# Optimization experiments

Hardware: AMD Instinct MI355X
Metric: run time of the kernel (lower is better)

The kernel has to match this reference:

```python
import jax, jax.numpy as jnp
import numpy as np

NUM_BITS = 8
MAX_INT = 2 ** (NUM_BITS - 1) - 1   # 127
MIN_INT = -2 ** (NUM_BITS - 1) - 1  # -129 (faithful to source)


def setup_inputs() -> dict:
    key = jax.random.key(0)
    k1, k2 = jax.random.split(key)
    B, H, S, D = 2, 16, 2048, 128
    score = jax.random.normal(k1, (B, H, S, S), dtype=jnp.float32)
    value = jax.random.normal(k2, (B, H, S, D), dtype=jnp.float32)
    query_scale = jnp.array([0.05], dtype=jnp.float32)
    key_scale = jnp.array([0.02], dtype=jnp.float32)
    return {"score": score, "value": value,
            "query_scale": query_scale, "key_scale": key_scale}


def _fake_quant(x, scale):
    # round(x/scale) then clamp to [MIN_INT, MAX_INT]
    return jnp.clip(jnp.round(x / scale), MIN_INT, MAX_INT)


def reference(score, value, query_scale, key_scale):
    # score: [B,H,S,S], value: [B,H,S,D]
    score_int = _fake_quant(score, query_scale)
    value_int = _fake_quant(value, key_scale)
    # integer-valued matmul (done in float here, as in the torch source)
    output_int = jnp.einsum('bhsk,bhkd->bhsd', score_int, value_int)
    final_scale = query_scale * key_scale
    return output_int * final_scale
```

## Files before the change

### kernel.cpp

```cpp
#include <hip/hip_runtime.h>
#include <hip/hip_bf16.h>
#include <stdint.h>

#define S_DIM 2048
#define D_DIM 128
#define BH_N  32
#define BM    64
#define BK    64
#define ASTR  72

typedef float  f32x4  __attribute__((ext_vector_type(4)));
typedef unsigned int u32x2 __attribute__((ext_vector_type(2)));
typedef unsigned int u32x4 __attribute__((ext_vector_type(4)));
typedef short  bf16x8 __attribute__((ext_vector_type(8)));

__device__ __forceinline__ unsigned short quant1(float v, float inv) {
    float q = rintf(v * inv);
    q = fminf(fmaxf(q, -129.0f), 127.0f);
    return (unsigned short)(__float_as_uint(q) >> 16);
}

__global__ __launch_bounds__(256) void vt_quant_kernel(
        const float* __restrict__ value,
        const float* __restrict__ ks_p,
        unsigned short* __restrict__ vt) {
    __shared__ unsigned short T[D_DIM * ASTR];

    const int bid = blockIdx.x;
    const int bh  = bid >> 5;
    const int k0  = (bid & 31) * BK;
    const float inv = 1.0f / ks_p[0];
    const int tid = threadIdx.x;

    const float* src = value + ((size_t)bh * S_DIM + k0) * D_DIM;

#pragma unroll
    for (int i = 0; i < 8; ++i) {
        int f  = tid + 256 * i;
        int k  = f >> 5;
        int c4 = (f & 31) * 4;
        f32x4 v = *(const f32x4*)(src + (size_t)k * D_DIM + c4);
        T[(c4 + 0) * ASTR + k] = quant1(v.x, inv);
        T[(c4 + 1) * ASTR + k] = quant1(v.y, inv);
        T[(c4 + 2) * ASTR + k] = quant1(v.z, inv);
        T[(c4 + 3) * ASTR + k] = quant1(v.w, inv);
    }
    __syncthreads();

    unsigned short* dst = vt + (size_t)bh * D_DIM * S_DIM + k0;
#pragma unroll
    for (int i = 0; i < 4; ++i) {
        int c = tid + 256 * i;
        int n = c >> 3;
        int q = (c & 7) * 8;
        u32x4 x = *(const u32x4*)(&T[n * ASTR + q]);
        *(u32x4*)(dst + (size_t)n * S_DIM + q) = x;
    }
}

__global__ __launch_bounds__(256, 4) void bmm_kernel(
        const float* __restrict__ score,
        const unsigned short* __restrict__ vt,
        const float* __restrict__ qs_p,
        const float* __restrict__ ks_p,
        float* __restrict__ out) {
    __shared__ unsigned short As[BM * ASTR];
    __shared__ unsigned short Bs[D_DIM * BK];

    const int bid = blockIdx.x;
    const int bh  = bid >> 5;
    const int m0  = (bid & 31) * BM;

    const float qs  = qs_p[0];
    const float inv_qs = 1.0f / qs;
    const float fin = qs * ks_p[0];

    const int tid  = threadIdx.x;
    const int lane = tid & 63;
    const int wave = tid >> 6;
    const int wm   = (wave >> 1) * 32;
    const int wn   = (wave & 1) * 64;
    const int m16  = lane & 15;
    const int quad = lane >> 4;

    const float* A = score + (size_t)bh * S_DIM * S_DIM + (size_t)m0 * S_DIM;
    const unsigned short* Bt = vt + (size_t)bh * D_DIM * S_DIM;

    f32x4 acc[2][4] = {};

    for (int kb = 0; kb < S_DIM; kb += BK) {
#pragma unroll
        for (int i = 0; i < 4; ++i) {
            int p  = i * 256 + tid;
            int n  = p >> 3;
            int ql = (p & 7) ^ (n & 7);
            const unsigned short* g = Bt + (size_t)n * S_DIM + kb + ql * 8;
            __builtin_amdgcn_global_load_lds(
                (const __attribute__((address_space(1))) void*)g,
                (__attribute__((address_space(3))) void*)(Bs + p * 8),
                16, 0, 0);
        }
#pragma unroll
        for (int i = 0; i < 4; ++i) {
            int f = tid + 256 * i;
            int r = f >> 4;
            int c = (f & 15) * 4;
            f32x4 v = __builtin_nontemporal_load(
                (const f32x4*)(A + (size_t)r * S_DIM + kb + c));
            unsigned int w0 = (unsigned int)quant1(v.x, inv_qs) |
                              ((unsigned int)quant1(v.y, inv_qs) << 16);
            unsigned int w1 = (unsigned int)quant1(v.z, inv_qs) |
                              ((unsigned int)quant1(v.w, inv_qs) << 16);
            u32x2 wv; wv.x = w0; wv.y = w1;
            *(u32x2*)(&As[r * ASTR + c]) = wv;
        }
        __syncthreads();

#pragma unroll
        for (int kk = 0; kk < BK; kk += 32) {
            bf16x8 af[2], bf[4];
#pragma unroll
            for (int i = 0; i < 2; ++i)
                af[i] = *(const bf16x8*)(&As[(wm + i * 16 + m16) * ASTR + kk + quad * 8]);
#pragma unroll
            for (int j = 0; j < 4; ++j) {
                int n  = wn + j * 16 + m16;
                int ch = ((kk >> 3) + quad) ^ (n & 7);
                bf[j] = *(const bf16x8*)(&Bs[(n * 8 + ch) * 8]);
            }
#pragma unroll
            for (int i = 0; i < 2; ++i)
#pragma unroll
                for (int j = 0; j < 4; ++j)
                    acc[i][j] = __builtin_amdgcn_mfma_f32_16x16x32_bf16(
                        af[i], bf[j], acc[i][j], 0, 0, 0);
        }
        __syncthreads();
    }

    float* O = out + (size_t)bh * S_DIM * D_DIM
                   + (size_t)(m0 + wm + quad * 4) * D_DIM + wn + m16;
#pragma unroll
    for (int i = 0; i < 2; ++i)
#pragma unroll
        for (int r = 0; r < 4; ++r)
#pragma unroll
            for (int j = 0; j < 4; ++j)
                O[(size_t)(i * 16 + r) * D_DIM + j * 16] = acc[i][j][r] * fin;
}

extern "C" void kernel_launch(void* const* d_in, const int* in_sizes, int n_in,
                              void* d_out, int out_size, void* d_ws, size_t ws_size,
                              hipStream_t stream) {
    const float* score = (const float*)d_in[0];
    const float* value = (const float*)d_in[1];
    const float* qs    = (const float*)d_in[2];
    const float* ks    = (const float*)d_in[3];
    float* out = (float*)d_out;
    unsigned short* vt = (unsigned short*)d_ws;

    vt_quant_kernel<<<BH_N * (S_DIM / BK), 256, 0, stream>>>(value, ks, vt);
    bmm_kernel<<<BH_N * (S_DIM / BM), 256, 0, stream>>>(score, vt, qs, ks, out);
}
```

Measured before the change: 718.9 us.

## Drop LDS staging; load score and Vt fragments directly into MFMA registers

Each wave now loads its 16 rows of score straight from global memory, quantizes them in registers, and reads Vt fragments directly from global/L2 instead of staging both through shared memory with barriers. Block indices are remapped so consecutive blocks span different batch-heads, and the occupancy hint in the launch bounds is removed. This removes LDS traffic and __syncthreads stalls from a memory-bound loop. In exchange, every wave reloads the full Vt tile from cache, and the per-lane strided score loads may coalesce worse.

```diff
diff --git a/kernel.cpp b/kernel.cpp
--- a/kernel.cpp
+++ b/kernel.cpp
@@ -10,7 +10,6 @@
 #define ASTR  72
 
 typedef float  f32x4  __attribute__((ext_vector_type(4)));
-typedef unsigned int u32x2 __attribute__((ext_vector_type(2)));
 typedef unsigned int u32x4 __attribute__((ext_vector_type(4)));
 typedef short  bf16x8 __attribute__((ext_vector_type(8)));
 
@@ -18,6 +17,15 @@
     float q = rintf(v * inv);
     q = fminf(fmaxf(q, -129.0f), 127.0f);
     return (unsigned short)(__float_as_uint(q) >> 16);
+}
+
+__device__ __forceinline__ bf16x8 quant8(f32x4 a, f32x4 b, float inv) {
+    bf16x8 r;
+    r[0] = (short)quant1(a.x, inv); r[1] = (short)quant1(a.y, inv);
+    r[2] = (short)quant1(a.z, inv); r[3] = (short)quant1(a.w, inv);
+    r[4] = (short)quant1(b.x, inv); r[5] = (short)quant1(b.y, inv);
+    r[6] = (short)quant1(b.z, inv); r[7] = (short)quant1(b.w, inv);
+    return r;
 }
 
 __global__ __launch_bounds__(256) void vt_quant_kernel(
@@ -58,95 +66,54 @@
     }
 }
 
-__global__ __launch_bounds__(256, 4) void bmm_kernel(
+__global__ __launch_bounds__(256) void bmm_kernel(
         const float* __restrict__ score,
         const unsigned short* __restrict__ vt,
         const float* __restrict__ qs_p,
         const float* __restrict__ ks_p,
         float* __restrict__ out) {
-    __shared__ unsigned short As[BM * ASTR];
-    __shared__ unsigned short Bs[D_DIM * BK];
+    const int bid = blockIdx.x;
+    const int bh  = (bid & 7) * 4 + (bid >> 8);
+    const int m0  = ((bid >> 3) & 31) * BM;
 
-    const int bid = blockIdx.x;
-    const int bh  = bid >> 5;
-    const int m0  = (bid & 31) * BM;
-
-    const float qs  = qs_p[0];
-    const float inv_qs = 1.0f / qs;
-    const float fin = qs * ks_p[0];
+    const float inv_qs = 1.0f / qs_p[0];
+    const float fin = qs_p[0] * ks_p[0];
 
     const int tid  = threadIdx.x;
     const int lane = tid & 63;
     const int wave = tid >> 6;
-    const int wm   = (wave >> 1) * 32;
-    const int wn   = (wave & 1) * 64;
     const int m16  = lane & 15;
     const int quad = lane >> 4;
 
-    const float* A = score + (size_t)bh * S_DIM * S_DIM + (size_t)m0 * S_DIM;
-    const unsigned short* Bt = vt + (size_t)bh * D_DIM * S_DIM;
+    const float* Ar = score + (size_t)bh * S_DIM * S_DIM
+                            + (size_t)(m0 + wave * 16 + m16) * S_DIM;
+    const unsigned short* Br = vt + (size_t)bh * D_DIM * S_DIM
+                                  + (size_t)m16 * S_DIM;
 
-    f32x4 acc[2][4] = {};
+    f32x4 acc[8] = {};
 
     for (int kb = 0; kb < S_DIM; kb += BK) {
 #pragma unroll
-        for (int i = 0; i < 4; ++i) {
-            int p  = i * 256 + tid;
-            int n  = p >> 3;
-            int ql = (p & 7) ^ (n & 7);
-            const unsigned short* g = Bt + (size_t)n * S_DIM + kb + ql * 8;
-            __builtin_amdgcn_global_load_lds(
-                (const __attribute__((address_space(1))) void*)g,
-                (__attribute__((address_space(3))) void*)(Bs + p * 8),
-                16, 0, 0);
+        for (int kk = 0; kk < BK; kk += 32) {
+            const int ko = kb + kk + quad * 8;
+            f32x4 a0 = __builtin_nontemporal_load((const f32x4*)(Ar + ko));
+            f32x4 a1 = __builtin_nontemporal_load((const f32x4*)(Ar + ko + 4));
+            bf16x8 af = quant8(a0, a1, inv_qs);
+#pragma unroll
+            for (int j = 0; j < 8; ++j) {
+                bf16x8 bf = *(const bf16x8*)(Br + (size_t)(j * 16) * S_DIM + ko);
+                acc[j] = __builtin_amdgcn_mfma_f32_16x16x32_bf16(af, bf, acc[j], 0, 0, 0);
+            }
         }
-#pragma unroll
-        for (int i = 0; i < 4; ++i) {
-            int f = tid + 256 * i;
-            int r = f >> 4;
-            int c = (f & 15) * 4;
-            f32x4 v = __builtin_nontemporal_load(
-                (const f32x4*)(A + (size_t)r * S_DIM + kb + c));
-            unsigned int w0 = (unsigned int)quant1(v.x, inv_qs) |
-                              ((unsigned int)quant1(v.y, inv_qs) << 16);
-            unsigned int w1 = (unsigned int)quant1(v.z, inv_qs) |
-                              ((unsigned int)quant1(v.w, inv_qs) << 16);
-            u32x2 wv; wv.x = w0; wv.y = w1;
-            *(u32x2*)(&As[r * ASTR + c]) = wv;
-        }
-        __syncthreads();
-
-#pragma unroll
-        for (int kk = 0; kk < BK; kk += 32) {
-            bf16x8 af[2], bf[4];
-#pragma unroll
-            for (int i = 0; i < 2; ++i)
-                af[i] = *(const bf16x8*)(&As[(wm + i * 16 + m16) * ASTR + kk + quad * 8]);
-#pragma unroll
-            for (int j = 0; j < 4; ++j) {
-                int n  = wn + j * 16 + m16;
-                int ch = ((kk >> 3) + quad) ^ (n & 7);
-                bf[j] = *(const bf16x8*)(&Bs[(n * 8 + ch) * 8]);
-            }
-#pragma unroll
-            for (int i = 0; i < 2; ++i)
-#pragma unroll
-                for (int j = 0; j < 4; ++j)
-                    acc[i][j] = __builtin_amdgcn_mfma_f32_16x16x32_bf16(
-                        af[i], bf[j], acc[i][j], 0, 0, 0);
-        }
-        __syncthreads();
     }
 
     float* O = out + (size_t)bh * S_DIM * D_DIM
-                   + (size_t)(m0 + wm + quad * 4) * D_DIM + wn + m16;
+                   + (size_t)(m0 + wave * 16 + quad * 4) * D_DIM + m16;
 #pragma unroll
-    for (int i = 0; i < 2; ++i)
+    for (int j = 0; j < 8; ++j)
 #pragma unroll
         for (int r = 0; r < 4; ++r)
-#pragma unroll
-            for (int j = 0; j < 4; ++j)
-                O[(size_t)(i * 16 + r) * D_DIM + j * 16] = acc[i][j][r] * fin;
+            O[(size_t)r * D_DIM + j * 16] = acc[j][r] * fin;
 }
 
 extern "C" void kernel_launch(void* const* d_in, const int* in_sizes, int n_in,
```

New measurement: 910.6 us. 1.27x slower.
